# Kernel tuning notes

Hardware: AMD Instinct MI355X
Metric: run time of the kernel (lower is better)

The kernel has to match this reference:

```python
import jax, jax.numpy as jnp
import numpy as np

B, N, F = 4, 4096, 6
K = 8
EPS = 1e-3  # keras BatchNormalization default epsilon


def _dense_params(key, fan_in, fan_out):
    lim = np.sqrt(6.0 / (fan_in + fan_out))
    w = jax.random.uniform(key, (fan_in, fan_out), jnp.float32, -lim, lim)
    return w, jnp.zeros((fan_out,), jnp.float32)


def setup_inputs() -> dict:
    key = jax.random.key(0)
    ks = jax.random.split(key, 12)
    inp = {}
    inp["inputs"] = jax.random.normal(ks[0], (B, N, F), jnp.float32)
    # BatchNorm 1 (over F channels), inference-mode moving stats
    inp["bn1_gamma"] = jnp.ones((F,), jnp.float32)
    inp["bn1_beta"] = jnp.zeros((F,), jnp.float32)
    inp["bn1_mean"] = jnp.zeros((F,), jnp.float32)
    inp["bn1_var"] = jnp.ones((F,), jnp.float32)
    # GravNet1 MLP: Dense(F-2 -> 32, relu), Dense(32 -> 32)
    inp["g1_w1"], inp["g1_b1"] = _dense_params(ks[1], F - 2, 32)
    inp["g1_w2"], inp["g1_b2"] = _dense_params(ks[2], 32, 32)
    # GravNet2 MLP: Dense(32 -> 32, relu), Dense(32 -> 32)
    inp["g2_w1"], inp["g2_b1"] = _dense_params(ks[3], 32, 32)
    inp["g2_w2"], inp["g2_b2"] = _dense_params(ks[4], 32, 32)
    # trailing dense stack: concat(x1, x2) has dim 34+34 = 68
    inp["d1_w"], inp["d1_b"] = _dense_params(ks[5], 68, 128)
    inp["d2_w"], inp["d2_b"] = _dense_params(ks[6], 128, 64)
    inp["d3_w"], inp["d3_b"] = _dense_params(ks[7], 64, 32)
    inp["bn2_gamma"] = jnp.ones((32,), jnp.float32)
    inp["bn2_beta"] = jnp.zeros((32,), jnp.float32)
    inp["bn2_mean"] = jnp.zeros((32,), jnp.float32)
    inp["bn2_var"] = jnp.ones((32,), jnp.float32)
    inp["out_w"], inp["out_b"] = _dense_params(ks[8], 32, 1)
    return inp


def _batchnorm(x, gamma, beta, mean, var):
    return (x - mean) * jax.lax.rsqrt(var + EPS) * gamma + beta


def _gravnet(x, w1, b1, w2, b2):
    pos, feat = x[..., :2], x[..., 2:]              # [B,N,2], [B,N,Fd]
    diff = pos[:, :, None, :] - pos[:, None, :, :]  # [B,N,N,2]
    d2 = jnp.sum(diff * diff, axis=-1)              # squared dist: same ordering as tf.norm
    _, idx = jax.lax.top_k(-d2, K + 1)              # ascending-distance indices
    idx = idx[..., 1:]                              # drop self -> [B,N,K]
    nb = jax.vmap(lambda f, i: f[i])(feat, idx)     # gather, batch_dims=1 -> [B,N,K,Fd]
    agg = jnp.mean(nb, axis=-2)                     # [B,N,Fd]
    h = jax.nn.relu(agg @ w1 + b1) @ w2 + b2        # MLP -> [B,N,32]
    return jnp.concatenate([pos, h], axis=-1)       # [B,N,34]


def reference(inputs, bn1_gamma, bn1_beta, bn1_mean, bn1_var,
              g1_w1, g1_b1, g1_w2, g1_b2,
              g2_w1, g2_b1, g2_w2, g2_b2,
              d1_w, d1_b, d2_w, d2_b, d3_w, d3_b,
              bn2_gamma, bn2_beta, bn2_mean, bn2_var,
              out_w, out_b):
    x = _batchnorm(inputs, bn1_gamma, bn1_beta, bn1_mean, bn1_var)
    x1 = _gravnet(x, g1_w1, g1_b1, g1_w2, g1_b2)
    x2 = _gravnet(x1, g2_w1, g2_b1, g2_w2, g2_b2)
    x = jnp.concatenate([x1, x2], axis=-1)          # [B,N,68]
    x = jax.nn.relu(x @ d1_w + d1_b)
    x = jax.nn.relu(x @ d2_w + d2_b)
    x = jax.nn.relu(x @ d3_w + d3_b)
    x = _batchnorm(x, bn2_gamma, bn2_beta, bn2_mean, bn2_var)
    return x @ out_w + out_b                        # [B,N,1]
```

## Files before the change

kernel.cpp:

```cpp
#include <hip/hip_runtime.h>
#include <hip/hip_bf16.h>

#define BTOT 4
#define NPTS 4096
#define FTOT 6
#define KNN 8
#define EPSV 1e-3f

__device__ __forceinline__ unsigned long long shfl_xor_u64(unsigned long long v, int mask) {
    unsigned lo = (unsigned)v, hi = (unsigned)(v >> 32);
    lo = (unsigned)__shfl_xor((int)lo, mask);
    hi = (unsigned)__shfl_xor((int)hi, mask);
    return ((unsigned long long)hi << 32) | lo;
}

__global__ __launch_bounds__(256) void k_bn1(const float* __restrict__ in,
                                             const float* __restrict__ g,
                                             const float* __restrict__ b,
                                             const float* __restrict__ m,
                                             const float* __restrict__ v,
                                             float* __restrict__ x,
                                             float2* __restrict__ pos) {
    int i = blockIdx.x * 256 + threadIdx.x;
    if (i >= BTOT * NPTS) return;
    float o[FTOT];
#pragma unroll
    for (int f = 0; f < FTOT; ++f) {
        float val = in[(size_t)i * FTOT + f];
        o[f] = (val - m[f]) * rsqrtf(v[f] + EPSV) * g[f] + b[f];
        x[(size_t)i * FTOT + f] = o[f];
    }
    pos[i] = make_float2(o[0], o[1]);
}

__global__ __launch_bounds__(512) void k_knn(const float2* __restrict__ posg,
                                             int* __restrict__ idx) {
    __shared__ float2 spos[NPTS];
    int b  = blockIdx.x >> 8;
    int q0 = (blockIdx.x & 255) << 4;
    int t  = threadIdx.x;
    const float2* pb = posg + (size_t)b * NPTS;
    for (int j = t; j < NPTS; j += 512) spos[j] = pb[j];
    __syncthreads();

    int lq = t >> 5;
    int p  = t & 31;
    int qq = q0 + lq;
    float2 q = spos[qq];

    unsigned long long bm0 = ~0ULL, bm1 = ~0ULL, bm2 = ~0ULL, bm3 = ~0ULL;
    for (int jj = 0; jj < NPTS / 32; jj += 4) {
        int j0 = ((jj + 0) << 5) + p;
        int j1 = ((jj + 1) << 5) + p;
        int j2 = ((jj + 2) << 5) + p;
        int j3 = ((jj + 3) << 5) + p;
        float2 p0 = spos[j0], p1 = spos[j1], p2 = spos[j2], p3 = spos[j3];
        float d0 = __fadd_rn(__fmul_rn(q.x - p0.x, q.x - p0.x), __fmul_rn(q.y - p0.y, q.y - p0.y));
        float d1 = __fadd_rn(__fmul_rn(q.x - p1.x, q.x - p1.x), __fmul_rn(q.y - p1.y, q.y - p1.y));
        float d2 = __fadd_rn(__fmul_rn(q.x - p2.x, q.x - p2.x), __fmul_rn(q.y - p2.y, q.y - p2.y));
        float d3 = __fadd_rn(__fmul_rn(q.x - p3.x, q.x - p3.x), __fmul_rn(q.y - p3.y, q.y - p3.y));
        unsigned long long k0 = ((unsigned long long)__float_as_uint(d0) << 32) | (unsigned)j0;
        unsigned long long k1 = ((unsigned long long)__float_as_uint(d1) << 32) | (unsigned)j1;
        unsigned long long k2 = ((unsigned long long)__float_as_uint(d2) << 32) | (unsigned)j2;
        unsigned long long k3 = ((unsigned long long)__float_as_uint(d3) << 32) | (unsigned)j3;
        bm0 = k0 < bm0 ? k0 : bm0;
        bm1 = k1 < bm1 ? k1 : bm1;
        bm2 = k2 < bm2 ? k2 : bm2;
        bm3 = k3 < bm3 ? k3 : bm3;
    }
    unsigned long long bma = bm0 < bm1 ? bm0 : bm1;
    unsigned long long bmb = bm2 < bm3 ? bm2 : bm3;
    unsigned long long bm  = bma < bmb ? bma : bmb;

    unsigned long long KK = bm, r = 0;
#pragma unroll
    for (int rd = 0; rd < 9; ++rd) {
        unsigned long long mn = KK;
#pragma unroll
        for (int s = 1; s <= 16; s <<= 1) {
            unsigned long long o = shfl_xor_u64(mn, s);
            mn = (o < mn) ? o : mn;
        }
        if (KK == mn) KK = ~0ULL;
        r = mn;
    }
    unsigned long long sent = r + 1;

    unsigned long long K[9];
#pragma unroll
    for (int m = 0; m < 9; ++m) K[m] = sent;

#pragma unroll 4
    for (int jj = 0; jj < NPTS / 32; ++jj) {
        int j = (jj << 5) + p;
        float2 pt = spos[j];
        float dx = q.x - pt.x;
        float dy = q.y - pt.y;
        float d2 = __fadd_rn(__fmul_rn(dx, dx), __fmul_rn(dy, dy));
        unsigned long long key = ((unsigned long long)__float_as_uint(d2) << 32) | (unsigned)j;
        if (key < K[8]) {
            K[8] = key;
#pragma unroll
            for (int m = 8; m > 0; --m) {
                bool sw = K[m] < K[m - 1];
                unsigned long long a = sw ? K[m - 1] : K[m];
                unsigned long long c = sw ? K[m] : K[m - 1];
                K[m] = a; K[m - 1] = c;
            }
        }
    }

    int rec = qq;
#pragma unroll
    for (int rd = 0; rd < 9; ++rd) {
        unsigned long long mn = K[0];
#pragma unroll
        for (int s = 1; s <= 16; s <<= 1) {
            unsigned long long o = shfl_xor_u64(mn, s);
            mn = (o < mn) ? o : mn;
        }
        if (K[0] == mn) {
#pragma unroll
            for (int i = 0; i < 8; ++i) K[i] = K[i + 1];
            K[8] = ~0ULL;
        }
        if (rd >= 1 && p == rd - 1) rec = (int)(unsigned)mn;
    }
    rec &= (NPTS - 1);
    if (p < 8)
        idx[((size_t)b * NPTS + qq) * KNN + p] = rec;
}

__global__ __launch_bounds__(64) void k_g1(const float* __restrict__ x,
                                           const int* __restrict__ idx,
                                           const float* __restrict__ w1,
                                           const float* __restrict__ b1,
                                           const float* __restrict__ w2,
                                           const float* __restrict__ b2,
                                           float* __restrict__ xcat) {
    __shared__ float sw1[4 * 32], sw2[32 * 32], sb1[32], sb2[32];
    int t = threadIdx.x;
    for (int u = t; u < 128; u += 64) sw1[u] = w1[u];
    for (int u = t; u < 1024; u += 64) sw2[u] = w2[u];
    if (t < 32) { sb1[t] = b1[t]; sb2[t] = b2[t]; }
    __syncthreads();

    int i = blockIdx.x * 64 + t;
    int b = i >> 12;
    int n = i & (NPTS - 1);
    const float* xb = x + (size_t)b * NPTS * FTOT;

    float agg[4] = {0.f, 0.f, 0.f, 0.f};
#pragma unroll
    for (int k = 0; k < KNN; ++k) {
        int nb = idx[(size_t)i * KNN + k];
        const float* f = xb + (size_t)nb * FTOT + 2;
        agg[0] += f[0]; agg[1] += f[1]; agg[2] += f[2]; agg[3] += f[3];
    }
#pragma unroll
    for (int k = 0; k < 4; ++k) agg[k] *= 0.125f;

    float h[32];
#pragma unroll
    for (int o = 0; o < 32; ++o) {
        float a = sb1[o];
#pragma unroll
        for (int k = 0; k < 4; ++k) a += agg[k] * sw1[k * 32 + o];
        h[o] = fmaxf(a, 0.f);
    }
    float* oc = xcat + (size_t)i * 68;
    oc[0] = xb[(size_t)n * FTOT];
    oc[1] = xb[(size_t)n * FTOT + 1];
#pragma unroll
    for (int o = 0; o < 32; ++o) {
        float a = sb2[o];
#pragma unroll
        for (int k = 0; k < 32; ++k) a += h[k] * sw2[k * 32 + o];
        oc[2 + o] = a;
    }
}

__global__ __launch_bounds__(64) void k_g2(float* __restrict__ xcat,
                                           const int* __restrict__ idx,
                                           const float* __restrict__ w1,
                                           const float* __restrict__ b1,
                                           const float* __restrict__ w2,
                                           const float* __restrict__ b2) {
    __shared__ float sw1[32 * 32], sw2[32 * 32], sb1[32], sb2[32];
    int t = threadIdx.x;
    for (int u = t; u < 1024; u += 64) { sw1[u] = w1[u]; sw2[u] = w2[u]; }
    if (t < 32) { sb1[t] = b1[t]; sb2[t] = b2[t]; }
    __syncthreads();

    int i = blockIdx.x * 64 + t;
    int b = i >> 12;

    float agg[32];
#pragma unroll
    for (int j = 0; j < 32; ++j) agg[j] = 0.f;
#pragma unroll
    for (int k = 0; k < KNN; ++k) {
        int nb = idx[(size_t)i * KNN + k];
        const float* f = xcat + ((size_t)b * NPTS + nb) * 68 + 2;
#pragma unroll
        for (int j = 0; j < 32; ++j) agg[j] += f[j];
    }
#pragma unroll
    for (int j = 0; j < 32; ++j) agg[j] *= 0.125f;

    float h[32];
#pragma unroll
    for (int o = 0; o < 32; ++o) {
        float a = sb1[o];
#pragma unroll
        for (int k = 0; k < 32; ++k) a += agg[k] * sw1[k * 32 + o];
        h[o] = fmaxf(a, 0.f);
    }
    float* oc = xcat + (size_t)i * 68;
    oc[34] = oc[0];
    oc[35] = oc[1];
#pragma unroll
    for (int o = 0; o < 32; ++o) {
        float a = sb2[o];
#pragma unroll
        for (int k = 0; k < 32; ++k) a += h[k] * sw2[k * 32 + o];
        oc[36 + o] = a;
    }
}

__global__ __launch_bounds__(256) void k_mlp(const float* __restrict__ xcat,
                                             const float* __restrict__ w1, const float* __restrict__ b1,
                                             const float* __restrict__ w2, const float* __restrict__ b2,
                                             const float* __restrict__ w3, const float* __restrict__ b3,
                                             const float* __restrict__ g,  const float* __restrict__ be,
                                             const float* __restrict__ mn, const float* __restrict__ vr,
                                             const float* __restrict__ ow, const float* __restrict__ ob,
                                             float* __restrict__ out) {
    __shared__ float xT[68][36];
    __shared__ float h1T[128][36];
    __shared__ float h2T[64][36];
    int t = threadIdx.x;
    int base = blockIdx.x * 32;

    for (int u = t; u < 32 * 68; u += 256) {
        int p = u / 68, k = u - p * 68;
        xT[k][p] = xcat[(size_t)(base + p) * 68 + k];
    }
    __syncthreads();

    int pq = t & 7;
    int oq = t >> 3;

    {
        const float* bp = b1 + 4 * oq;
        float4 a0 = make_float4(bp[0], bp[0], bp[0], bp[0]);
        float4 a1 = make_float4(bp[1], bp[1], bp[1], bp[1]);
        float4 a2 = make_float4(bp[2], bp[2], bp[2], bp[2]);
        float4 a3 = make_float4(bp[3], bp[3], bp[3], bp[3]);
#pragma unroll 4
        for (int k = 0; k < 68; ++k) {
            float4 xv = *(const float4*)&xT[k][4 * pq];
            const float* wr = w1 + (size_t)k * 128 + 4 * oq;
            float w0v = wr[0], w1v = wr[1], w2v = wr[2], w3v = wr[3];
            a0.x += w0v * xv.x; a0.y += w0v * xv.y; a0.z += w0v * xv.z; a0.w += w0v * xv.w;
            a1.x += w1v * xv.x; a1.y += w1v * xv.y; a1.z += w1v * xv.z; a1.w += w1v * xv.w;
            a2.x += w2v * xv.x; a2.y += w2v * xv.y; a2.z += w2v * xv.z; a2.w += w2v * xv.w;
            a3.x += w3v * xv.x; a3.y += w3v * xv.y; a3.z += w3v * xv.z; a3.w += w3v * xv.w;
        }
        a0.x = fmaxf(a0.x, 0.f); a0.y = fmaxf(a0.y, 0.f); a0.z = fmaxf(a0.z, 0.f); a0.w = fmaxf(a0.w, 0.f);
        a1.x = fmaxf(a1.x, 0.f); a1.y = fmaxf(a1.y, 0.f); a1.z = fmaxf(a1.z, 0.f); a1.w = fmaxf(a1.w, 0.f);
        a2.x = fmaxf(a2.x, 0.f); a2.y = fmaxf(a2.y, 0.f); a2.z = fmaxf(a2.z, 0.f); a2.w = fmaxf(a2.w, 0.f);
        a3.x = fmaxf(a3.x, 0.f); a3.y = fmaxf(a3.y, 0.f); a3.z = fmaxf(a3.z, 0.f); a3.w = fmaxf(a3.w, 0.f);
        *(float4*)&h1T[4 * oq + 0][4 * pq] = a0;
        *(float4*)&h1T[4 * oq + 1][4 * pq] = a1;
        *(float4*)&h1T[4 * oq + 2][4 * pq] = a2;
        *(float4*)&h1T[4 * oq + 3][4 * pq] = a3;
    }
    __syncthreads();

    if (t < 128) {
        const float* bp = b2 + 4 * oq;
        float4 a0 = make_float4(bp[0], bp[0], bp[0], bp[0]);
        float4 a1 = make_float4(bp[1], bp[1], bp[1], bp[1]);
        float4 a2 = make_float4(bp[2], bp[2], bp[2], bp[2]);
        float4 a3 = make_float4(bp[3], bp[3], bp[3], bp[3]);
#pragma unroll 4
        for (int k = 0; k < 128; ++k) {
            float4 xv = *(const float4*)&h1T[k][4 * pq];
            const float* wr = w2 + (size_t)k * 64 + 4 * oq;
            float w0v = wr[0], w1v = wr[1], w2v = wr[2], w3v = wr[3];
            a0.x += w0v * xv.x; a0.y += w0v * xv.y; a0.z += w0v * xv.z; a0.w += w0v * xv.w;
            a1.x += w1v * xv.x; a1.y += w1v * xv.y; a1.z += w1v * xv.z; a1.w += w1v * xv.w;
            a2.x += w2v * xv.x; a2.y += w2v * xv.y; a2.z += w2v * xv.z; a2.w += w2v * xv.w;
            a3.x += w3v * xv.x; a3.y += w3v * xv.y; a3.z += w3v * xv.z; a3.w += w3v * xv.w;
        }
        a0.x = fmaxf(a0.x, 0.f); a0.y = fmaxf(a0.y, 0.f); a0.z = fmaxf(a0.z, 0.f); a0.w = fmaxf(a0.w, 0.f);
        a1.x = fmaxf(a1.x, 0.f); a1.y = fmaxf(a1.y, 0.f); a1.z = fmaxf(a1.z, 0.f); a1.w = fmaxf(a1.w, 0.f);
        a2.x = fmaxf(a2.x, 0.f); a2.y = fmaxf(a2.y, 0.f); a2.z = fmaxf(a2.z, 0.f); a2.w = fmaxf(a2.w, 0.f);
        a3.x = fmaxf(a3.x, 0.f); a3.y = fmaxf(a3.y, 0.f); a3.z = fmaxf(a3.z, 0.f); a3.w = fmaxf(a3.w, 0.f);
        *(float4*)&h2T[4 * oq + 0][4 * pq] = a0;
        *(float4*)&h2T[4 * oq + 1][4 * pq] = a1;
        *(float4*)&h2T[4 * oq + 2][4 * pq] = a2;
        *(float4*)&h2T[4 * oq + 3][4 * pq] = a3;
    }
    __syncthreads();

    if (t < 64) {
        const float* bp = b3 + 4 * oq;
        float4 a0 = make_float4(bp[0], bp[0], bp[0], bp[0]);
        float4 a1 = make_float4(bp[1], bp[1], bp[1], bp[1]);
        float4 a2 = make_float4(bp[2], bp[2], bp[2], bp[2]);
        float4 a3 = make_float4(bp[3], bp[3], bp[3], bp[3]);
#pragma unroll 4
        for (int k = 0; k < 64; ++k) {
            float4 xv = *(const float4*)&h2T[k][4 * pq];
            const float* wr = w3 + (size_t)k * 32 + 4 * oq;
            float w0v = wr[0], w1v = wr[1], w2v = wr[2], w3v = wr[3];
            a0.x += w0v * xv.x; a0.y += w0v * xv.y; a0.z += w0v * xv.z; a0.w += w0v * xv.w;
            a1.x += w1v * xv.x; a1.y += w1v * xv.y; a1.z += w1v * xv.z; a1.w += w1v * xv.w;
            a2.x += w2v * xv.x; a2.y += w2v * xv.y; a2.z += w2v * xv.z; a2.w += w2v * xv.w;
            a3.x += w3v * xv.x; a3.y += w3v * xv.y; a3.z += w3v * xv.z; a3.w += w3v * xv.w;
        }
        a0.x = fmaxf(a0.x, 0.f); a0.y = fmaxf(a0.y, 0.f); a0.z = fmaxf(a0.z, 0.f); a0.w = fmaxf(a0.w, 0.f);
        a1.x = fmaxf(a1.x, 0.f); a1.y = fmaxf(a1.y, 0.f); a1.z = fmaxf(a1.z, 0.f); a1.w = fmaxf(a1.w, 0.f);
        a2.x = fmaxf(a2.x, 0.f); a2.y = fmaxf(a2.y, 0.f); a2.z = fmaxf(a2.z, 0.f); a2.w = fmaxf(a2.w, 0.f);
        a3.x = fmaxf(a3.x, 0.f); a3.y = fmaxf(a3.y, 0.f); a3.z = fmaxf(a3.z, 0.f); a3.w = fmaxf(a3.w, 0.f);
        int c0 = 4 * oq;
        float s0 = g[c0 + 0] * rsqrtf(vr[c0 + 0] + EPSV);
        float s1 = g[c0 + 1] * rsqrtf(vr[c0 + 1] + EPSV);
        float s2 = g[c0 + 2] * rsqrtf(vr[c0 + 2] + EPSV);
        float s3 = g[c0 + 3] * rsqrtf(vr[c0 + 3] + EPSV);
        float w0 = s0 * ow[c0 + 0], w1c = s1 * ow[c0 + 1];
        float w2c = s2 * ow[c0 + 2], w3c = s3 * ow[c0 + 3];
        float tt = (be[c0 + 0] - mn[c0 + 0] * s0) * ow[c0 + 0]
                 + (be[c0 + 1] - mn[c0 + 1] * s1) * ow[c0 + 1]
                 + (be[c0 + 2] - mn[c0 + 2] * s2) * ow[c0 + 2]
                 + (be[c0 + 3] - mn[c0 + 3] * s3) * ow[c0 + 3];
        float4 s;
        s.x = a0.x * w0 + a1.x * w1c + a2.x * w2c + a3.x * w3c;
        s.y = a0.y * w0 + a1.y * w1c + a2.y * w2c + a3.y * w3c;
        s.z = a0.z * w0 + a1.z * w1c + a2.z * w2c + a3.z * w3c;
        s.w = a0.w * w0 + a1.w * w1c + a2.w * w2c + a3.w * w3c;
#pragma unroll
        for (int msk = 8; msk <= 32; msk <<= 1) {
            s.x += __shfl_xor(s.x, msk);
            s.y += __shfl_xor(s.y, msk);
            s.z += __shfl_xor(s.z, msk);
            s.w += __shfl_xor(s.w, msk);
            tt  += __shfl_xor(tt,  msk);
        }
        if (oq == 0) {
            float c = tt + ob[0];
            *(float4*)(out + base + 4 * pq) = make_float4(s.x + c, s.y + c, s.z + c, s.w + c);
        }
    }
}

extern "C" void kernel_launch(void* const* d_in, const int* in_sizes, int n_in,
                              void* d_out, int out_size, void* d_ws, size_t ws_size,
                              hipStream_t stream) {
    const float* inputs    = (const float*)d_in[0];
    const float* bn1_gamma = (const float*)d_in[1];
    const float* bn1_beta  = (const float*)d_in[2];
    const float* bn1_mean  = (const float*)d_in[3];
    const float* bn1_var   = (const float*)d_in[4];
    const float* g1_w1 = (const float*)d_in[5];
    const float* g1_b1 = (const float*)d_in[6];
    const float* g1_w2 = (const float*)d_in[7];
    const float* g1_b2 = (const float*)d_in[8];
    const float* g2_w1 = (const float*)d_in[9];
    const float* g2_b1 = (const float*)d_in[10];
    const float* g2_w2 = (const float*)d_in[11];
    const float* g2_b2 = (const float*)d_in[12];
    const float* d1_w = (const float*)d_in[13];
    const float* d1_b = (const float*)d_in[14];
    const float* d2_w = (const float*)d_in[15];
    const float* d2_b = (const float*)d_in[16];
    const float* d3_w = (const float*)d_in[17];
    const float* d3_b = (const float*)d_in[18];
    const float* bn2_gamma = (const float*)d_in[19];
    const float* bn2_beta  = (const float*)d_in[20];
    const float* bn2_mean  = (const float*)d_in[21];
    const float* bn2_var   = (const float*)d_in[22];
    const float* out_w = (const float*)d_in[23];
    const float* out_b = (const float*)d_in[24];
    float* out = (float*)d_out;

    const size_t BN = (size_t)BTOT * NPTS;
    char* ws = (char*)d_ws;
    size_t off = 0;
    auto alloc = [&](size_t bytes) { char* p = ws + off; off += (bytes + 255) & ~(size_t)255; return p; };
    float*  x    = (float*) alloc(BN * FTOT * sizeof(float));
    float2* pos  = (float2*)alloc(BN * sizeof(float2));
    int*    idx  = (int*)   alloc(BN * KNN  * sizeof(int));
    float*  xcat = (float*) alloc(BN * 68   * sizeof(float));
    (void)ws_size; (void)n_in; (void)in_sizes; (void)out_size;

    k_bn1<<<dim3(64),   dim3(256), 0, stream>>>(inputs, bn1_gamma, bn1_beta, bn1_mean, bn1_var, x, pos);
    k_knn<<<dim3(1024), dim3(512), 0, stream>>>(pos, idx);
    k_g1 <<<dim3(256),  dim3(64),  0, stream>>>(x, idx, g1_w1, g1_b1, g1_w2, g1_b2, xcat);
    k_g2 <<<dim3(256),  dim3(64),  0, stream>>>(xcat, idx, g2_w1, g2_b1, g2_w2, g2_b2);
    k_mlp<<<dim3(512),  dim3(256), 0, stream>>>(xcat, d1_w, d1_b, d2_w, d2_b, d3_w, d3_b,
                                                bn2_gamma, bn2_beta, bn2_mean, bn2_var,
                                                out_w, out_b, out);
}
```

Before: 109.4 us.

## Split each GravNet point across four threads with shuffle-based feature exchange

k_g1 and k_g2 now give each point four threads instead of one. Each thread gathers a quarter of the neighbour features and computes eight of the 32 MLP outputs, and wavefront shuffles share the aggregated and hidden vectors among the four lanes. Shared weight arrays are padded to a stride of 33, and k_g2 loads features as float2. The aim is more in-flight threads (256 blocks of 256 threads instead of 64) and less per-thread register pressure and serial FMA work. In exchange it adds shuffle traffic and redundant per-point index loads.

New measurement: 104.0 us. 4.9% less time.

```diff
diff --git a/kernel.cpp b/kernel.cpp
--- a/kernel.cpp
+++ b/kernel.cpp
@@ -131,100 +131,146 @@
         idx[((size_t)b * NPTS + qq) * KNN + p] = rec;
 }
 
-__global__ __launch_bounds__(64) void k_g1(const float* __restrict__ x,
-                                           const int* __restrict__ idx,
-                                           const float* __restrict__ w1,
-                                           const float* __restrict__ b1,
-                                           const float* __restrict__ w2,
-                                           const float* __restrict__ b2,
-                                           float* __restrict__ xcat) {
-    __shared__ float sw1[4 * 32], sw2[32 * 32], sb1[32], sb2[32];
+__global__ __launch_bounds__(256) void k_g1(const float* __restrict__ x,
+                                            const int* __restrict__ idx,
+                                            const float* __restrict__ w1,
+                                            const float* __restrict__ b1,
+                                            const float* __restrict__ w2,
+                                            const float* __restrict__ b2,
+                                            float* __restrict__ xcat) {
+    __shared__ float sw1[4 * 33], sw2[32 * 33], sb1[32], sb2[32];
     int t = threadIdx.x;
-    for (int u = t; u < 128; u += 64) sw1[u] = w1[u];
-    for (int u = t; u < 1024; u += 64) sw2[u] = w2[u];
+    if (t < 128) sw1[(t >> 5) * 33 + (t & 31)] = w1[t];
+    for (int u = t; u < 1024; u += 256) sw2[(u >> 5) * 33 + (u & 31)] = w2[u];
     if (t < 32) { sb1[t] = b1[t]; sb2[t] = b2[t]; }
     __syncthreads();
 
-    int i = blockIdx.x * 64 + t;
+    int i = blockIdx.x * 64 + (t >> 2);
+    int s = t & 3;
+    int qb = (t & 63) & ~3;
     int b = i >> 12;
     int n = i & (NPTS - 1);
     const float* xb = x + (size_t)b * NPTS * FTOT;
 
-    float agg[4] = {0.f, 0.f, 0.f, 0.f};
+    float aggs = 0.f;
 #pragma unroll
     for (int k = 0; k < KNN; ++k) {
         int nb = idx[(size_t)i * KNN + k];
-        const float* f = xb + (size_t)nb * FTOT + 2;
-        agg[0] += f[0]; agg[1] += f[1]; agg[2] += f[2]; agg[3] += f[3];
-    }
-#pragma unroll
-    for (int k = 0; k < 4; ++k) agg[k] *= 0.125f;
-
-    float h[32];
-#pragma unroll
-    for (int o = 0; o < 32; ++o) {
-        float a = sb1[o];
-#pragma unroll
-        for (int k = 0; k < 4; ++k) a += agg[k] * sw1[k * 32 + o];
-        h[o] = fmaxf(a, 0.f);
-    }
+        aggs += xb[(size_t)nb * FTOT + 2 + s];
+    }
+    aggs *= 0.125f;
+
+    float af0 = __shfl(aggs, qb + 0);
+    float af1 = __shfl(aggs, qb + 1);
+    float af2 = __shfl(aggs, qb + 2);
+    float af3 = __shfl(aggs, qb + 3);
+
+    int o0 = 8 * s;
+    float h[8];
+#pragma unroll
+    for (int u = 0; u < 8; ++u) {
+        int o = o0 + u;
+        float a = af0 * sw1[0 * 33 + o] + af1 * sw1[1 * 33 + o]
+                + af2 * sw1[2 * 33 + o] + af3 * sw1[3 * 33 + o];
+        h[u] = fmaxf(a + sb1[o], 0.f);
+    }
+
+    float hf[32];
+#pragma unroll
+    for (int w = 0; w < 4; ++w)
+#pragma unroll
+        for (int u = 0; u < 8; ++u)
+            hf[8 * w + u] = __shfl(h[u], qb + w);
+
     float* oc = xcat + (size_t)i * 68;
-    oc[0] = xb[(size_t)n * FTOT];
-    oc[1] = xb[(size_t)n * FTOT + 1];
-#pragma unroll
-    for (int o = 0; o < 32; ++o) {
-        float a = sb2[o];
-#pragma unroll
-        for (int k = 0; k < 32; ++k) a += h[k] * sw2[k * 32 + o];
-        oc[2 + o] = a;
-    }
-}
-
-__global__ __launch_bounds__(64) void k_g2(float* __restrict__ xcat,
-                                           const int* __restrict__ idx,
-                                           const float* __restrict__ w1,
-                                           const float* __restrict__ b1,
-                                           const float* __restrict__ w2,
-                                           const float* __restrict__ b2) {
-    __shared__ float sw1[32 * 32], sw2[32 * 32], sb1[32], sb2[32];
+    if (s == 0) {
+        oc[0] = xb[(size_t)n * FTOT];
+        oc[1] = xb[(size_t)n * FTOT + 1];
+    }
+#pragma unroll
+    for (int u = 0; u < 8; ++u) {
+        int o = o0 + u;
+        float a = 0.f;
+#pragma unroll
+        for (int k = 0; k < 32; ++k) a += hf[k] * sw2[k * 33 + o];
+        oc[2 + o] = a + sb2[o];
+    }
+}
+
+__global__ __launch_bounds__(256) void k_g2(float* __restrict__ xcat,
+                                            const int* __restrict__ idx,
+                                            const float* __restrict__ w1,
+                                            const float* __restrict__ b1,
+                                            const float* __restrict__ w2,
+                                            const float* __restrict__ b2) {
+    __shared__ float sw1[32 * 33], sw2[32 * 33], sb1[32], sb2[32];
     int t = threadIdx.x;
-    for (int u = t; u < 1024; u += 64) { sw1[u] = w1[u]; sw2[u] = w2[u]; }
+    for (int u = t; u < 1024; u += 256) {
+        sw1[(u >> 5) * 33 + (u & 31)] = w1[u];
+        sw2[(u >> 5) * 33 + (u & 31)] = w2[u];
+    }
     if (t < 32) { sb1[t] = b1[t]; sb2[t] = b2[t]; }
     __syncthreads();
 
-    int i = blockIdx.x * 64 + t;
+    int i = blockIdx.x * 64 + (t >> 2);
+    int s = t & 3;
+    int qb = (t & 63) & ~3;
     int b = i >> 12;
 
-    float agg[32];
-#pragma unroll
-    for (int j = 0; j < 32; ++j) agg[j] = 0.f;
+    float agg[8];
+#pragma unroll
+    for (int u = 0; u < 8; ++u) agg[u] = 0.f;
 #pragma unroll
     for (int k = 0; k < KNN; ++k) {
         int nb = idx[(size_t)i * KNN + k];
-        const float* f = xcat + ((size_t)b * NPTS + nb) * 68 + 2;
-#pragma unroll
-        for (int j = 0; j < 32; ++j) agg[j] += f[j];
-    }
-#pragma unroll
-    for (int j = 0; j < 32; ++j) agg[j] *= 0.125f;
-
-    float h[32];
-#pragma unroll
-    for (int o = 0; o < 32; ++o) {
-        float a = sb1[o];
-#pragma unroll
-        for (int k = 0; k < 32; ++k) a += agg[k] * sw1[k * 32 + o];
-        h[o] = fmaxf(a, 0.f);
-    }
+        const float2* f2 = (const float2*)(xcat + ((size_t)b * NPTS + nb) * 68 + 2 + 8 * s);
+#pragma unroll
+        for (int w = 0; w < 4; ++w) {
+            float2 a = f2[w];
+            agg[2 * w]     += a.x;
+            agg[2 * w + 1] += a.y;
+        }
+    }
+#pragma unroll
+    for (int u = 0; u < 8; ++u) agg[u] *= 0.125f;
+
+    float af[32];
+#pragma unroll
+    for (int w = 0; w < 4; ++w)
+#pragma unroll
+        for (int u = 0; u < 8; ++u)
+            af[8 * w + u] = __shfl(agg[u], qb + w);
+
+    int o0 = 8 * s;
+    float h[8];
+#pragma unroll
+    for (int u = 0; u < 8; ++u) {
+        int o = o0 + u;
+        float a = 0.f;
+#pragma unroll
+        for (int k = 0; k < 32; ++k) a += af[k] * sw1[k * 33 + o];
+        h[u] = fmaxf(a + sb1[o], 0.f);
+    }
+
+    float hf[32];
+#pragma unroll
+    for (int w = 0; w < 4; ++w)
+#pragma unroll
+        for (int u = 0; u < 8; ++u)
+            hf[8 * w + u] = __shfl(h[u], qb + w);
+
     float* oc = xcat + (size_t)i * 68;
-    oc[34] = oc[0];
-    oc[35] = oc[1];
-#pragma unroll
-    for (int o = 0; o < 32; ++o) {
-        float a = sb2[o];
-#pragma unroll
-        for (int k = 0; k < 32; ++k) a += h[k] * sw2[k * 32 + o];
-        oc[36 + o] = a;
+    if (s == 0) {
+        oc[34] = oc[0];
+        oc[35] = oc[1];
+    }
+#pragma unroll
+    for (int u = 0; u < 8; ++u) {
+        int o = o0 + u;
+        float a = 0.f;
+#pragma unroll
+        for (int k = 0; k < 32; ++k) a += hf[k] * sw2[k * 33 + o];
+        oc[36 + o] = a + sb2[o];
     }
 }
 
@@ -398,8 +444,8 @@
 
     k_bn1<<<dim3(64),   dim3(256), 0, stream>>>(inputs, bn1_gamma, bn1_beta, bn1_mean, bn1_var, x, pos);
     k_knn<<<dim3(1024), dim3(512), 0, stream>>>(pos, idx);
-    k_g1 <<<dim3(256),  dim3(64),  0, stream>>>(x, idx, g1_w1, g1_b1, g1_w2, g1_b2, xcat);
-    k_g2 <<<dim3(256),  dim3(64),  0, stream>>>(xcat, idx, g2_w1, g2_b1, g2_w2, g2_b2);
+    k_g1 <<<dim3(256),  dim3(256), 0, stream>>>(x, idx, g1_w1, g1_b1, g1_w2, g1_b2, xcat);
+    k_g2 <<<dim3(256),  dim3(256), 0, stream>>>(xcat, idx, g2_w1, g2_b1, g2_w2, g2_b2);
     k_mlp<<<dim3(512),  dim3(256), 0, stream>>>(xcat, d1_w, d1_b, d2_w, d2_b, d3_w, d3_b,
                                                 bn2_gamma, bn2_beta, bn2_mean, bn2_var,
                                                 out_w, out_b, out);
```
